# Kernel optimization log

Measured on AMD Instinct MI355X. Metric: run time of the kernel, lower is better.

## Reference

```python
import jax, jax.numpy as jnp
import numpy as np

# flattened layer dilations for blocks [[1,3],[6,12]]
DILATIONS = [1, 3, 6, 12]
BLOCK_LAYERS = [[0, 1], [2, 3]]
H_SIZE = 64
STATE_SIZE = 128
OUT_SIZE = STATE_SIZE - H_SIZE  # 64


def _s2_layer(x_seq, W, b, d):
    """Run one S2Cell layer with dilation d over a full sequence.
    x_seq: [T, B, in], W: [4*state, in+2*h], b: [4*state]. Returns [T, B, OUT_SIZE].
    Keeps a circular buffer of the last d (h, c) states so the delayed state
    at step t is the state from step t-d (buffer slot t mod d, read before write).
    """
    T, B, _ = x_seq.shape

    def step(carry, inp):
        prevH, prevC, hbuf, cbuf = carry
        xt, t = inp
        idx = jnp.mod(t, d)
        dH = jax.lax.dynamic_index_in_dim(hbuf, idx, axis=0, keepdims=False)
        dC = jax.lax.dynamic_index_in_dim(cbuf, idx, axis=0, keepdims=False)
        hasPrev = t > 0
        hasDel = t >= d
        # no prev state -> zeros for both h slots; prev but no delayed -> prevH twice
        prevH_u = jnp.where(hasPrev, prevH, 0.0)
        dH_u = jnp.where(hasDel, dH, prevH_u)
        xh = jnp.concatenate([xt, prevH_u, dH_u], axis=1)  # [B, in+2h]
        gates = xh @ W.T + b  # [B, 4*state]
        g0, g1, g2, g3 = jnp.split(gates, 4, axis=1)
        f = jax.nn.sigmoid(g0 + 1.0)
        ns = jnp.tanh(g1)
        alpha = jax.nn.sigmoid(g2)
        o = jax.nn.sigmoid(g3)
        wC = jnp.where(hasDel, alpha * prevC + (1.0 - alpha) * dC, prevC)
        newC = jnp.where(hasPrev, f * wC + (1.0 - f) * ns, ns)
        whole = o * newC  # [B, state]
        out = whole[:, :OUT_SIZE]
        h = whole[:, OUT_SIZE:]
        hbuf = jax.lax.dynamic_update_index_in_dim(hbuf, h, idx, axis=0)
        cbuf = jax.lax.dynamic_update_index_in_dim(cbuf, newC, idx, axis=0)
        return (h, newC, hbuf, cbuf), out

    carry0 = (jnp.zeros((B, H_SIZE), x_seq.dtype),
              jnp.zeros((B, STATE_SIZE), x_seq.dtype),
              jnp.zeros((d, B, H_SIZE), x_seq.dtype),
              jnp.zeros((d, B, STATE_SIZE), x_seq.dtype))
    _, ys = jax.lax.scan(step, carry0, (x_seq, jnp.arange(T)))
    return ys


def setup_inputs() -> dict:
    key = jax.random.key(0)
    ks = jax.random.split(key, 4)
    T, B = 256, 256
    x = jax.random.normal(ks[0], (T, B, 64), dtype=jnp.float32)
    W = jax.random.normal(ks[1], (4, 4 * STATE_SIZE, 64 + 2 * H_SIZE), dtype=jnp.float32) * 0.08
    b = jnp.zeros((4, 4 * STATE_SIZE), dtype=jnp.float32)
    Wa = jax.random.normal(ks[2], (64, OUT_SIZE), dtype=jnp.float32) * 0.1
    ba = jnp.zeros((64,), dtype=jnp.float32)
    return {"x": x, "W": W, "b": b, "Wa": Wa, "ba": ba}


def reference(x, W, b, Wa, ba):
    T, B, _ = x.shape
    prevBlockOut = jnp.zeros((T, B, OUT_SIZE), x.dtype)
    for bi, block in enumerate(BLOCK_LAYERS):
        h = x if bi == 0 else prevBlockOut
        for li in block:
            h = _s2_layer(h, W[li], b[li], DILATIONS[li])
        prevBlockOut = h + prevBlockOut  # residual across blocks
    return prevBlockOut @ Wa.T + ba  # [T, B, output_size]
```

## Files before the change

### kernel.cpp

```cpp
#include <hip/hip_runtime.h>
#include <cmath>

#define TT 256
#define KD 192
#define RINGM 127

typedef _Float16 f16;
typedef _Float16 f16x4 __attribute__((ext_vector_type(4)));
typedef _Float16 f16x8 __attribute__((ext_vector_type(8)));
typedef float    f32x4 __attribute__((ext_vector_type(4)));
typedef unsigned int u32;

#define SWZ(b,k) ((k) ^ (((b)&7)<<3))
#define MFMA16(a,bb,c) __builtin_amdgcn_mfma_f32_16x16x32_f16((a),(bb),(c),0,0,0)

__device__ __forceinline__ float sigm(float x){
  return __builtin_amdgcn_rcpf(1.0f + __expf(-x));
}
__device__ __forceinline__ float ftanh(float x){
  x = fminf(15.0f, fmaxf(-15.0f, x));
  float e = __expf(-2.0f*x);
  return (1.0f - e) * __builtin_amdgcn_rcpf(1.0f + e);
}
__device__ __forceinline__ void waitflag(const u32* p, u32 v){
  while (__hip_atomic_load(p, __ATOMIC_ACQUIRE, __HIP_MEMORY_SCOPE_AGENT) != v)
    __builtin_amdgcn_s_sleep(2);
}
__device__ __forceinline__ void setflag(u32* p, u32 v){
  __hip_atomic_store(p, v, __ATOMIC_RELEASE, __HIP_MEMORY_SCOPE_AGENT);
}

extern "C" __global__ void
__attribute__((amdgpu_flat_work_group_size(512,512), amdgpu_waves_per_eu(2,2)))
s2_pipe_kernel(const float* __restrict__ xin, const float* __restrict__ W,
               const float* __restrict__ bias, const float* __restrict__ Wa,
               const float* __restrict__ ba, float* __restrict__ out,
               f16* __restrict__ bufA, f16* __restrict__ bufC,
               u32* __restrict__ fwdf, u32* __restrict__ consf)
{
  const int tid  = threadIdx.x;
  const int wave = tid >> 6;
  const int lane = tid & 63;
  const int b    = lane & 15;
  const int g4   = lane >> 4;
  const int bg   = blockIdx.x & 15;
  const int l    = blockIdx.x >> 4;
  const int gb   = bg*16 + b;
  const int s0   = wave*16 + g4*4;
  const int d    = (l==0)?1:((l==1)?3:((l==2)?6:12));

  __shared__ f16 sxh[2][16*KD];
  __shared__ f16 scb[12*16*128];
  __shared__ f16 shb[12*16*64];
  __shared__ f16 sfin[2][16*64];

  u32* fIn  = fwdf + (((l>0)?(l-1):0)*16 + bg)*64;
  u32* fOut = fwdf + (((l<3)?l:0)*16 + bg)*64;
  u32* cPub = consf + (((l==3)?1:0)*16 + bg)*64;
  u32* cPol = consf + (((l==2)?1:0)*16 + bg)*64;
  f16* ringOut       = (l==0) ? bufA : bufC;
  const f16* ringIn  = (l==1) ? bufA : bufC;

  f16x8 aP[2]; f32x4 cbP;
  if (l==3 && wave < 4) {
    #pragma unroll
    for (int kt=0;kt<2;++kt) {
      const float* p = Wa + (size_t)(wave*16 + b)*64 + kt*32 + g4*8;
      float4 lo = *(const float4*)p, hi = *(const float4*)(p+4);
      f16x8 v;
      v[0]=(f16)lo.x; v[1]=(f16)lo.y; v[2]=(f16)lo.z; v[3]=(f16)lo.w;
      v[4]=(f16)hi.x; v[5]=(f16)hi.y; v[6]=(f16)hi.z; v[7]=(f16)hi.w;
      aP[kt]=v;
    }
    float4 bb4 = *(const float4*)(ba + s0);
    cbP[0]=bb4.x; cbP[1]=bb4.y; cbP[2]=bb4.z; cbP[3]=bb4.w;
  }

  f16x8 aW[4][6]; f32x4 cb[4];
  const float* Wl = W + (size_t)l*512*KD;
  #pragma unroll
  for (int q=0;q<4;++q) {
    const float* pr = Wl + (size_t)(128*q + 16*wave + b)*KD + g4*8;
    #pragma unroll
    for (int kt=0;kt<6;++kt) {
      float4 lo = *(const float4*)(pr + kt*32);
      float4 hi = *(const float4*)(pr + kt*32 + 4);
      f16x8 v;
      v[0]=(f16)lo.x; v[1]=(f16)lo.y; v[2]=(f16)lo.z; v[3]=(f16)lo.w;
      v[4]=(f16)hi.x; v[5]=(f16)hi.y; v[6]=(f16)hi.z; v[7]=(f16)hi.w;
      aW[q][kt]=v;
    }
    float4 b4 = *(const float4*)(bias + l*512 + 128*q + s0);
    cb[q][0]=b4.x; cb[q][1]=b4.y; cb[q][2]=b4.z; cb[q][3]=b4.w;
  }

  float4 xAf, xBf, skA, skB; f16x4 xAh, xBh;
  if (wave >= 4) {
    f16x4 zz = {(f16)0,(f16)0,(f16)0,(f16)0};
    *(f16x4*)&sxh[0][b*KD + SWZ(b, s0)]    = zz;
    *(f16x4*)&sxh[0][b*KD + SWZ(b, s0+64)] = zz;
  } else {
    if (l>0) waitflag(&fIn[0], 1u);
    if (l==0) {
      float4 v0 = *(const float4*)(xin + ((size_t)gb)*64 + s0);
      f16x4 h; h[0]=(f16)v0.x; h[1]=(f16)v0.y; h[2]=(f16)v0.z; h[3]=(f16)v0.w;
      *(f16x4*)&sxh[0][b*KD + SWZ(b, s0)] = h;
      xAf = *(const float4*)(xin + ((size_t)256 + gb)*64 + s0);
    } else if (l==2) {
      float4 v0 = *(const float4*)(out + ((size_t)gb)*64 + s0);
      f16x4 h; h[0]=(f16)v0.x; h[1]=(f16)v0.y; h[2]=(f16)v0.z; h[3]=(f16)v0.w;
      *(f16x4*)&sxh[0][b*KD + SWZ(b, s0)] = h;
      xAf = *(const float4*)(out + ((size_t)256 + gb)*64 + s0);
    } else {
      *(f16x4*)&sxh[0][b*KD + SWZ(b, s0)] =
          *(const f16x4*)(ringIn + ((size_t)0*256 + gb)*64 + s0);
      xAh = *(const f16x4*)(ringIn + ((size_t)1*256 + gb)*64 + s0);
      if (l==3) skA = *(const float4*)(out + ((size_t)gb)*64 + s0);
    }
  }
  float cpr[4] = {0.f,0.f,0.f,0.f};
  int idx = 0, ready = 0, consC = 0;
  __syncthreads();

  #pragma unroll 1
  for (int t=0; t<TT; ++t) {
    const int p = t & 1;
    const int idx2 = (idx+1==d) ? 0 : idx+1;

    f16x8 bx[6];
    const f16* xrow = &sxh[p][b*KD];
    #pragma unroll
    for (int kt=0;kt<6;++kt)
      bx[kt] = *(const f16x8*)&xrow[SWZ(b, kt*32 + g4*8)];

    f16x4 dCv = *(const f16x4*)&scb[(idx*16+b)*128 + SWZ(b, s0)];
    f16x4 dhE;
    if (wave >= 4 && d > 1)
      dhE = *(const f16x4*)&shb[(idx2*16+b)*64 + SWZ(b, s0-64)];

    if (wave < 4) {
      if (t+2 < TT) {
        int nc = (t+2) >> 2;
        if (l > 0 && nc > ready) { waitflag(&fIn[nc], (u32)(nc+1)); ready = nc; }
        if (l==0)      xBf = *(const float4*)(xin + ((size_t)(t+2)*256 + gb)*64 + s0);
        else if (l==2) xBf = *(const float4*)(out + ((size_t)(t+2)*256 + gb)*64 + s0);
        else           xBh = *(const f16x4*)(ringIn + ((size_t)((t+2)&RINGM)*256 + gb)*64 + s0);
      }
      if (l==3 && t+1 < TT) skB = *(const float4*)(out + ((size_t)(t+1)*256 + gb)*64 + s0);
      if ((l==0 || l==2) && (4*consC + 129 < t)) {
        int Ke = ((t-129+3)>>2) + 8; if (Ke > 64) Ke = 64;
        waitflag(&cPol[Ke-1], (u32)Ke);
        consC = Ke;
      }
    }

    if (l==3 && wave < 4 && t > 0) {
      const f16* fr = &sfin[p^1][b*64];
      f16x8 b0 = *(const f16x8*)&fr[SWZ(b, g4*8)];
      f16x8 b1 = *(const f16x8*)&fr[SWZ(b, 32 + g4*8)];
      f32x4 pa = cbP;
      pa = MFMA16(aP[0], b0, pa);
      pa = MFMA16(aP[1], b1, pa);
      float4 st; st.x=pa[0]; st.y=pa[1]; st.z=pa[2]; st.w=pa[3];
      *(float4*)(out + ((size_t)(t-1)*256 + gb)*64 + s0) = st;
    }

    f32x4 a0=cb[0], a1=cb[1], a2=cb[2], a3=cb[3];
    #pragma unroll
    for (int kt=0;kt<6;++kt) {
      a0 = MFMA16(aW[0][kt], bx[kt], a0);
      a1 = MFMA16(aW[1][kt], bx[kt], a1);
      a2 = MFMA16(aW[2][kt], bx[kt], a2);
      a3 = MFMA16(aW[3][kt], bx[kt], a3);
    }

    float whole[4]; f16x4 ncv;
    #pragma unroll
    for (int r=0;r<4;++r) {
      float f  = sigm(a0[r] + 1.0f);
      float ns = ftanh(a1[r]);
      float al = sigm(a2[r]);
      float o  = sigm(a3[r]);
      float dC = (float)dCv[r];
      float wC = (t>=d) ? fmaf(al, cpr[r]-dC, dC) : cpr[r];
      float nc = (t>0)  ? fmaf(f, wC-ns, ns) : ns;
      whole[r] = o*nc; cpr[r] = nc; ncv[r] = (f16)nc;
    }
    *(f16x4*)&scb[(idx*16+b)*128 + SWZ(b, s0)] = ncv;

    if (wave >= 4) {
      const int jj = s0 - 64;
      f16x4 hv;
      #pragma unroll
      for (int r=0;r<4;++r) hv[r]=(f16)whole[r];
      *(f16x4*)&shb[(idx*16+b)*64 + SWZ(b, jj)] = hv;
      *(f16x4*)&sxh[p^1][b*KD + SWZ(b, s0)] = hv;
      f16x4 dhv = hv;
      if (t+1 >= d && d > 1) dhv = dhE;
      *(f16x4*)&sxh[p^1][b*KD + SWZ(b, s0+64)] = dhv;
    } else {
      f16x4 xv;
      if (l==0 || l==2) { xv[0]=(f16)xAf.x; xv[1]=(f16)xAf.y; xv[2]=(f16)xAf.z; xv[3]=(f16)xAf.w; xAf = xBf; }
      else              { xv = xAh; xAh = xBh; }
      *(f16x4*)&sxh[p^1][b*KD + SWZ(b, s0)] = xv;
      if (l==3) {
        f16x4 fv;
        #pragma unroll
        for (int r=0;r<4;++r) fv[r] = (f16)(whole[r] + ((const float*)&skA)[r]);
        *(f16x4*)&sfin[p][b*64 + SWZ(b, s0)] = fv;
        skA = skB;
      } else if (l==1) {
        float4 st; st.x=whole[0]; st.y=whole[1]; st.z=whole[2]; st.w=whole[3];
        *(float4*)(out + ((size_t)t*256 + gb)*64 + s0) = st;
      } else {
        f16x4 ov;
        #pragma unroll
        for (int r=0;r<4;++r) ov[r]=(f16)whole[r];
        *(f16x4*)(ringOut + ((size_t)(t&RINGM)*256 + gb)*64 + s0) = ov;
      }
    }
    idx = idx2;
    __syncthreads();

    if ((t&3)==3 && tid==0) {
      if (l<3)            setflag(&fOut[t>>2], (u32)((t>>2)+1));
      if (l==1 || l==3)   setflag(&cPub[t>>2], (u32)((t>>2)+1));
    }
  }

  if (l==3 && wave < 4) {
    const f16* fr = &sfin[1][b*64];
    f16x8 b0 = *(const f16x8*)&fr[SWZ(b, g4*8)];
    f16x8 b1 = *(const f16x8*)&fr[SWZ(b, 32 + g4*8)];
    f32x4 pa = cbP;
    pa = MFMA16(aP[0], b0, pa);
    pa = MFMA16(aP[1], b1, pa);
    float4 st; st.x=pa[0]; st.y=pa[1]; st.z=pa[2]; st.w=pa[3];
    *(float4*)(out + ((size_t)(TT-1)*256 + gb)*64 + s0) = st;
  }
}

extern "C" void kernel_launch(void* const* d_in, const int* in_sizes, int n_in,
                              void* d_out, int out_size, void* d_ws, size_t ws_size,
                              hipStream_t stream)
{
  const float* x  = (const float*)d_in[0];
  const float* W  = (const float*)d_in[1];
  const float* bb = (const float*)d_in[2];
  const float* Wa = (const float*)d_in[3];
  const float* ba = (const float*)d_in[4];
  float* out = (float*)d_out;

  f16* bufA  = (f16*)d_ws;
  f16* bufC  = (f16*)((char*)d_ws + (4u<<20));
  u32* fwdf  = (u32*)((char*)d_ws + (8u<<20));
  u32* consf = (u32*)((char*)d_ws + (8u<<20) + 3*16*64*4);

  hipLaunchKernelGGL(s2_pipe_kernel, dim3(64), dim3(512), 0, stream,
                     x, W, bb, Wa, ba, out, bufA, bufC, fwdf, consf);
}
```

Baseline: 548.4 us.

## Use per-wave release flags and an LDS-only barrier in the layer pipeline

Each of the four producer waves now publishes its own progress and consumer flags right after the step barrier. Previously one thread did this after a full __syncthreads. Consumers poll all four per-wave flags, and the forward flag check is hoisted and made to look a few steps further ahead. The per-step __syncthreads is replaced by a barrier that waits only on LDS counters, so outstanding global loads and stores are not drained each step. The spin sleep is also shortened. The aim is to cut per-step barrier and signalling latency, at the cost of more flag polling and a longer required lead between pipeline stages.

```diff
diff --git a/kernel.cpp b/kernel.cpp
--- a/kernel.cpp
+++ b/kernel.cpp
@@ -14,6 +14,13 @@
 #define SWZ(b,k) ((k) ^ (((b)&7)<<3))
 #define MFMA16(a,bb,c) __builtin_amdgcn_mfma_f32_16x16x32_f16((a),(bb),(c),0,0,0)
 
+#define LBAR() do { \
+  __builtin_amdgcn_sched_barrier(0); \
+  asm volatile("s_waitcnt lgkmcnt(0)" ::: "memory"); \
+  __builtin_amdgcn_s_barrier(); \
+  __builtin_amdgcn_sched_barrier(0); \
+} while (0)
+
 __device__ __forceinline__ float sigm(float x){
   return __builtin_amdgcn_rcpf(1.0f + __expf(-x));
 }
@@ -24,7 +31,7 @@
 }
 __device__ __forceinline__ void waitflag(const u32* p, u32 v){
   while (__hip_atomic_load(p, __ATOMIC_ACQUIRE, __HIP_MEMORY_SCOPE_AGENT) != v)
-    __builtin_amdgcn_s_sleep(2);
+    __builtin_amdgcn_s_sleep(1);
 }
 __device__ __forceinline__ void setflag(u32* p, u32 v){
   __hip_atomic_store(p, v, __ATOMIC_RELEASE, __HIP_MEMORY_SCOPE_AGENT);
@@ -54,12 +61,14 @@
   __shared__ f16 shb[12*16*64];
   __shared__ f16 sfin[2][16*64];
 
-  u32* fIn  = fwdf + (((l>0)?(l-1):0)*16 + bg)*64;
-  u32* fOut = fwdf + (((l<3)?l:0)*16 + bg)*64;
-  u32* cPub = consf + (((l==3)?1:0)*16 + bg)*64;
-  u32* cPol = consf + (((l==2)?1:0)*16 + bg)*64;
-  f16* ringOut       = (l==0) ? bufA : bufC;
-  const f16* ringIn  = (l==1) ? bufA : bufC;
+  u32* myFwd = fwdf + (((l<3?l:0)*4 + (wave&3))*16 + bg)*64;
+  u32* fIn0  = fwdf + ((((l>0?l-1:0))*4 + 0)*16 + bg)*64;
+  const int pitch = 16*64;
+  u32* myCons = consf + ((((l==3)?1:0)*4 + (wave&3))*16 + bg)*64;
+  u32* cPol0  = consf + ((((l==2)?1:0)*4 + 0)*16 + bg)*64;
+
+  f16* ringOut      = (l==0) ? bufA : bufC;
+  const f16* ringIn = (l==1) ? bufA : bufC;
 
   f16x8 aP[2]; f32x4 cbP;
   if (l==3 && wave < 4) {
@@ -100,7 +109,10 @@
     *(f16x4*)&sxh[0][b*KD + SWZ(b, s0)]    = zz;
     *(f16x4*)&sxh[0][b*KD + SWZ(b, s0+64)] = zz;
   } else {
-    if (l>0) waitflag(&fIn[0], 1u);
+    if (l>0) {
+      #pragma unroll
+      for (int w=0;w<4;++w) waitflag(&fIn0[w*pitch + 0], 1u);
+    }
     if (l==0) {
       float4 v0 = *(const float4*)(xin + ((size_t)gb)*64 + s0);
       f16x4 h; h[0]=(f16)v0.x; h[1]=(f16)v0.y; h[2]=(f16)v0.z; h[3]=(f16)v0.w;
@@ -139,19 +151,31 @@
       dhE = *(const f16x4*)&shb[(idx2*16+b)*64 + SWZ(b, s0-64)];
 
     if (wave < 4) {
+      if (lane==0 && (t&3)==0 && t>0) {
+        const int g = (t>>2)-1; const u32 v = (u32)(t>>2);
+        if (l<3)          setflag(&myFwd[g], v);
+        if (l==1 || l==3) setflag(&myCons[g], v);
+      }
+      if ((l==0 || l==2) && (4*consC + 129 < t)) {
+        int Ke = ((t-129+3)>>2) + 8; if (Ke > 64) Ke = 64;
+        #pragma unroll
+        for (int w=0;w<4;++w) waitflag(&cPol0[w*pitch + Ke-1], (u32)Ke);
+        consC = Ke;
+      }
+      if (l > 0) {
+        int gk = (t+6)>>2; if (gk > 63) gk = 63;
+        if (gk > ready) {
+          #pragma unroll
+          for (int w=0;w<4;++w) waitflag(&fIn0[w*pitch + gk], (u32)(gk+1));
+          ready = gk;
+        }
+      }
       if (t+2 < TT) {
-        int nc = (t+2) >> 2;
-        if (l > 0 && nc > ready) { waitflag(&fIn[nc], (u32)(nc+1)); ready = nc; }
         if (l==0)      xBf = *(const float4*)(xin + ((size_t)(t+2)*256 + gb)*64 + s0);
         else if (l==2) xBf = *(const float4*)(out + ((size_t)(t+2)*256 + gb)*64 + s0);
         else           xBh = *(const f16x4*)(ringIn + ((size_t)((t+2)&RINGM)*256 + gb)*64 + s0);
       }
       if (l==3 && t+1 < TT) skB = *(const float4*)(out + ((size_t)(t+1)*256 + gb)*64 + s0);
-      if ((l==0 || l==2) && (4*consC + 129 < t)) {
-        int Ke = ((t-129+3)>>2) + 8; if (Ke > 64) Ke = 64;
-        waitflag(&cPol[Ke-1], (u32)Ke);
-        consC = Ke;
-      }
     }
 
     if (l==3 && wave < 4 && t > 0) {
@@ -220,12 +244,7 @@
       }
     }
     idx = idx2;
-    __syncthreads();
-
-    if ((t&3)==3 && tid==0) {
-      if (l<3)            setflag(&fOut[t>>2], (u32)((t>>2)+1));
-      if (l==1 || l==3)   setflag(&cPub[t>>2], (u32)((t>>2)+1));
-    }
+    LBAR();
   }
 
   if (l==3 && wave < 4) {
@@ -237,6 +256,11 @@
     pa = MFMA16(aP[1], b1, pa);
     float4 st; st.x=pa[0]; st.y=pa[1]; st.z=pa[2]; st.w=pa[3];
     *(float4*)(out + ((size_t)(TT-1)*256 + gb)*64 + s0) = st;
+  }
+
+  if (wave < 4 && lane == 0) {
+    if (l<3)          setflag(&myFwd[63], 64u);
+    if (l==1 || l==3) setflag(&myCons[63], 64u);
   }
 }
 
@@ -254,7 +278,7 @@
   f16* bufA  = (f16*)d_ws;
   f16* bufC  = (f16*)((char*)d_ws + (4u<<20));
   u32* fwdf  = (u32*)((char*)d_ws + (8u<<20));
-  u32* consf = (u32*)((char*)d_ws + (8u<<20) + 3*16*64*4);
+  u32* consf = (u32*)((char*)d_ws + (8u<<20) + 3*4*16*64*4);
 
   hipLaunchKernelGGL(s2_pipe_kernel, dim3(64), dim3(512), 0, stream,
                      x, W, bb, Wa, ba, out, bufA, bufC, fwdf, consf);
```

New measurement: 994.8 us. 1.81x slower.
